# Performance work log

Hardware: AMD Instinct MI355X
Metric: run time of the kernel (lower is better)

## Reference

```python
import jax, jax.numpy as jnp
import numpy as np

DIM = 768
HEADS = 12
HEAD_DIM = DIM // HEADS
HIDDEN = int(DIM * 4.0)
EPS = 1e-5


def _layernorm(x, g, b):
    mu = jnp.mean(x, axis=-1, keepdims=True)
    var = jnp.var(x, axis=-1, keepdims=True)
    return (x - mu) * jax.lax.rsqrt(var + EPS) * g + b


def setup_inputs() -> dict:
    key = jax.random.key(0)
    ks = jax.random.split(key, 12)
    s = 0.02
    return {
        "x": jax.random.normal(ks[0], (8, 1024, DIM), dtype=jnp.float32),
        "norm1_g": jnp.ones((DIM,), jnp.float32),
        "norm1_b": jnp.zeros((DIM,), jnp.float32),
        "qkv_w": jax.random.normal(ks[1], (3 * DIM, DIM), jnp.float32) * s,
        "qkv_b": jnp.zeros((3 * DIM,), jnp.float32),
        "proj_w": jax.random.normal(ks[2], (DIM, DIM), jnp.float32) * s,
        "proj_b": jnp.zeros((DIM,), jnp.float32),
        "norm2_g": jnp.ones((DIM,), jnp.float32),
        "norm2_b": jnp.zeros((DIM,), jnp.float32),
        "fc1_w": jax.random.normal(ks[3], (HIDDEN, DIM), jnp.float32) * s,
        "fc1_b": jnp.zeros((HIDDEN,), jnp.float32),
        "fc2_w": jax.random.normal(ks[4], (DIM, HIDDEN), jnp.float32) * s,
        "fc2_b": jnp.zeros((DIM,), jnp.float32),
    }


def reference(x, norm1_g, norm1_b, qkv_w, qkv_b, proj_w, proj_b,
              norm2_g, norm2_b, fc1_w, fc1_b, fc2_w, fc2_b):
    B, N, C = x.shape
    scale = HEAD_DIM ** -0.5

    # --- MHSA with pre-norm + residual ---
    h = _layernorm(x, norm1_g, norm1_b)
    qkv = h @ qkv_w.T + qkv_b                      # [B, N, 3C]
    qkv = qkv.reshape(B, N, 3, HEADS, HEAD_DIM)
    qkv = jnp.transpose(qkv, (2, 0, 3, 1, 4))      # [3, B, H, N, Dh]
    q, k, v = qkv[0], qkv[1], qkv[2]
    attn = jnp.einsum("bhnd,bhmd->bhnm", q, k) * scale
    attn = jax.nn.softmax(attn, axis=-1)
    o = jnp.einsum("bhnm,bhmd->bhnd", attn, v)     # [B, H, N, Dh]
    o = jnp.transpose(o, (0, 2, 1, 3)).reshape(B, N, C)
    x = x + (o @ proj_w.T + proj_b)

    # --- MLP with pre-norm + residual ---
    h = _layernorm(x, norm2_g, norm2_b)
    h = jax.nn.gelu(h @ fc1_w.T + fc1_b, approximate=False)
    x = x + (h @ fc2_w.T + fc2_b)
    return x
```

## Files before the change

kernel.cpp:

```cpp
#include <hip/hip_runtime.h>
#include <hip/hip_bf16.h>

typedef unsigned short u16;
using short8  = __attribute__((ext_vector_type(8))) short;
using floatx4 = __attribute__((ext_vector_type(4))) float;

__device__ inline u16 f2bu(float f) {
    __hip_bfloat16 h = __float2bfloat16(f);
    return __builtin_bit_cast(u16, h);
}
__device__ inline float b2f(u16 u) {
    unsigned v = (unsigned)u << 16;
    return __builtin_bit_cast(float, v);
}
__device__ inline float gelu_f(float v) {
    float u = 1.5957691216f * (v + 0.044715f * v * v * v);
    return v / (1.f + __expf(-u));
}

__device__ inline void load16(const u16* g, u16* l) {
    __builtin_amdgcn_global_load_lds(
        (const __attribute__((address_space(1))) void*)g,
        (__attribute__((address_space(3))) void*)l, 16, 0, 0);
}

__global__ void cvt_bf16v(const float4* __restrict__ in, ushort4* __restrict__ out, int n4) {
    int i = blockIdx.x * 256 + threadIdx.x;
    if (i < n4) {
        float4 f = in[i];
        ushort4 r;
        r.x = f2bu(f.x); r.y = f2bu(f.y); r.z = f2bu(f.z); r.w = f2bu(f.w);
        out[i] = r;
    }
}

__global__ __launch_bounds__(256) void layernorm_bf16(
    const float* __restrict__ x, const float* __restrict__ g,
    const float* __restrict__ b, u16* __restrict__ out)
{
    int row = blockIdx.x;
    int tid = threadIdx.x;
    const float* xr = x + (size_t)row * 768;
    float v0 = xr[tid], v1 = xr[tid + 256], v2 = xr[tid + 512];
    float s = v0 + v1 + v2;
    float ss = v0 * v0 + v1 * v1 + v2 * v2;
    for (int off = 1; off < 64; off <<= 1) {
        s  += __shfl_xor(s, off, 64);
        ss += __shfl_xor(ss, off, 64);
    }
    __shared__ float as[4], ass[4];
    int wave = tid >> 6, lane = tid & 63;
    if (lane == 0) { as[wave] = s; ass[wave] = ss; }
    __syncthreads();
    s  = as[0] + as[1] + as[2] + as[3];
    ss = ass[0] + ass[1] + ass[2] + ass[3];
    float mu  = s * (1.0f / 768.0f);
    float var = ss * (1.0f / 768.0f) - mu * mu;
    float rs  = rsqrtf(var + 1e-5f);
    u16* orow = out + (size_t)row * 768;
    orow[tid]       = f2bu((v0 - mu) * rs * g[tid]       + b[tid]);
    orow[tid + 256] = f2bu((v1 - mu) * rs * g[tid + 256] + b[tid + 256]);
    orow[tid + 512] = f2bu((v2 - mu) * rs * g[tid + 512] + b[tid + 512]);
}

__global__ __launch_bounds__(256) void red2(
    const ushort4* __restrict__ P0, const ushort4* __restrict__ P1,
    const float* __restrict__ bias, const float4* __restrict__ res,
    float4* __restrict__ out)
{
    int i = blockIdx.x * 256 + threadIdx.x;
    int col = (i % 192) * 4;
    ushort4 a = P0[i], b = P1[i];
    float4 o = res ? res[i] : out[i];
    o.x += bias[col + 0] + b2f(a.x) + b2f(b.x);
    o.y += bias[col + 1] + b2f(a.y) + b2f(b.y);
    o.z += bias[col + 2] + b2f(a.z) + b2f(b.z);
    o.w += bias[col + 3] + b2f(a.w) + b2f(b.w);
    out[i] = o;
}

__device__ inline void mfma_tile(const u16* lsa, const u16* lsb, int off,
                                 int wrow, int wcol, int l16, int xq,
                                 floatx4 acc[4][4])
{
    short8 af[4], bfr[4];
    #pragma unroll
    for (int rb = 0; rb < 4; ++rb) af[rb]  = *(const short8*)&lsa[off + (wrow + rb * 16 + l16) * 32 + xq];
    #pragma unroll
    for (int cb = 0; cb < 4; ++cb) bfr[cb] = *(const short8*)&lsb[off + (wcol + cb * 16 + l16) * 32 + xq];
    #pragma unroll
    for (int rb = 0; rb < 4; ++rb)
        #pragma unroll
        for (int cb = 0; cb < 4; ++cb)
            acc[rb][cb] = __builtin_amdgcn_mfma_f32_16x16x32_bf16(af[rb], bfr[cb], acc[rb][cb], 0, 0, 0);
}

__global__ __launch_bounds__(256) void gemm_pipe(
    const u16* __restrict__ A, int lda,
    const u16* __restrict__ B, int ldb,
    int K,
    const float* __restrict__ bias,
    const float* __restrict__ res,
    float* __restrict__ outf, u16* __restrict__ outb,
    u16* __restrict__ parts, size_t pstride,
    int ldc, int act, int splits)
{
    __shared__ u16 lsa[2 * 128 * 32];
    __shared__ u16 lsb[2 * 128 * 32];

    int tid  = threadIdx.x;
    int wave = tid >> 6, lane = tid & 63;
    int quad = lane >> 4, l16 = lane & 15;
    int wrow = (wave >> 1) * 64;
    int wcol = (wave & 1) * 64;

    int gx = gridDim.x;
    int nblk = gx * gridDim.y;
    int flat = blockIdx.y * gx + blockIdx.x;
    int d = (flat & 7) * (nblk >> 3) + (flat >> 3);
    int m0 = (d / gx) * 128, n0 = (d % gx) * 128;

    int Kper = K / splits;
    int kbeg = blockIdx.z * Kper;
    int nIter = Kper >> 5;

    floatx4 acc[4][4];
    for (int i = 0; i < 4; ++i)
        for (int j = 0; j < 4; ++j)
            acc[i][j] = (floatx4){0.f, 0.f, 0.f, 0.f};

    int srow = wave * 32 + (lane >> 2);
    int scol = (((lane & 3) ^ ((lane >> 3) & 3))) * 8;
    const u16* ga0 = A + (size_t)(m0 + srow)      * lda + kbeg + scol;
    const u16* ga1 = A + (size_t)(m0 + srow + 16) * lda + kbeg + scol;
    const u16* gb0 = B + (size_t)(n0 + srow)      * ldb + kbeg + scol;
    const u16* gb1 = B + (size_t)(n0 + srow + 16) * ldb + kbeg + scol;
    int wl0 = wave * 1024 + lane * 8;
    int wl1 = wl0 + 512;

    int xq = (quad ^ ((l16 >> 1) & 3)) * 8;

    uint4 A00, A01, B00, B01;
    uint4 A10, A11, B10, B11;

#define FETCH0() do { A00 = *(const uint4*)ga0; A01 = *(const uint4*)ga1; \
                      B00 = *(const uint4*)gb0; B01 = *(const uint4*)gb1; \
                      ga0 += 32; ga1 += 32; gb0 += 32; gb1 += 32; } while (0)
#define FETCH1() do { A10 = *(const uint4*)ga0; A11 = *(const uint4*)ga1; \
                      B10 = *(const uint4*)gb0; B11 = *(const uint4*)gb1; \
                      ga0 += 32; ga1 += 32; gb0 += 32; gb1 += 32; } while (0)
#define WRITE0(buf) do { *(uint4*)&lsa[(buf) + wl0] = A00; *(uint4*)&lsa[(buf) + wl1] = A01; \
                         *(uint4*)&lsb[(buf) + wl0] = B00; *(uint4*)&lsb[(buf) + wl1] = B01; } while (0)
#define WRITE1(buf) do { *(uint4*)&lsa[(buf) + wl0] = A10; *(uint4*)&lsa[(buf) + wl1] = A11; \
                         *(uint4*)&lsb[(buf) + wl0] = B10; *(uint4*)&lsb[(buf) + wl1] = B11; } while (0)

    FETCH0();
    FETCH1();
    WRITE0(0);
    __syncthreads();

    for (int it = 0; it < nIter; it += 2) {
        if (it + 2 < nIter) FETCH0();
        mfma_tile(lsa, lsb, 0, wrow, wcol, l16, xq, acc);
        WRITE1(4096);
        __syncthreads();
        if (it + 3 < nIter) FETCH1();
        mfma_tile(lsa, lsb, 4096, wrow, wcol, l16, xq, acc);
        if (it + 2 < nIter) WRITE0(0);
        __syncthreads();
    }
#undef FETCH0
#undef FETCH1
#undef WRITE0
#undef WRITE1

    u16* pdst = (splits > 1) ? parts + (size_t)blockIdx.z * pstride : nullptr;
    #pragma unroll
    for (int rb = 0; rb < 4; ++rb)
        #pragma unroll
        for (int cb = 0; cb < 4; ++cb)
            #pragma unroll
            for (int r = 0; r < 4; ++r) {
                int row = m0 + wrow + rb * 16 + quad * 4 + r;
                int col = n0 + wcol + cb * 16 + l16;
                float v = acc[rb][cb][r];
                if (splits > 1) {
                    pdst[(size_t)row * ldc + col] = f2bu(v);
                } else {
                    v += bias[col];
                    if (res) v += res[(size_t)row * ldc + col];
                    if (act) v = gelu_f(v);
                    if (outf) outf[(size_t)row * ldc + col] = v;
                    else      outb[(size_t)row * ldc + col] = f2bu(v);
                }
            }
}

__global__ __launch_bounds__(256) void attn_fused(
    const u16* __restrict__ qkv, u16* __restrict__ o)
{
    const int N = 1024, C3 = 2304;
    int qb = blockIdx.x;
    int bh = blockIdx.y;
    int b = bh / 12, h = bh % 12;
    int tid = threadIdx.x, wave = tid >> 6, lane = tid & 63;
    int quad = lane >> 4, l16 = lane & 15;

    __shared__ u16 lk[64 * 64];
    __shared__ u16 lvt[64][72];
    __shared__ u16 lp[4][16][72];

    const size_t base = (size_t)b * N * C3;
    int q0 = qb * 64 + wave * 16;

    short8 qa0 = *(const short8*)&qkv[base + (size_t)(q0 + l16) * C3 + h * 64 + quad * 8];
    short8 qa1 = *(const short8*)&qkv[base + (size_t)(q0 + l16) * C3 + h * 64 + 32 + quad * 8];

    floatx4 oacc[4];
    for (int i = 0; i < 4; ++i) oacc[i] = (floatx4){0.f, 0.f, 0.f, 0.f};
    float lsum[4] = {0.f, 0.f, 0.f, 0.f};

    for (int kt = 0; kt < N; kt += 64) {
        __syncthreads();
        #pragma unroll
        for (int i = 0; i < 2; ++i) {
            int idx = i * 2048 + wave * 512 + lane * 8;
            int r = idx >> 6;
            int gc = (lane & 7) ^ (r & 7);
            load16(&qkv[base + (size_t)(kt + r) * C3 + 768 + h * 64 + gc * 8], &lk[idx]);
        }
        {
            int key = tid & 63, dbase = (tid >> 6) * 16;
            const u16* vp = &qkv[base + (size_t)(kt + key) * C3 + 1536 + h * 64 + dbase];
            uint4 vv0 = *(const uint4*)vp;
            uint4 vv1 = *(const uint4*)(vp + 8);
            const u16* e0 = (const u16*)&vv0;
            const u16* e1 = (const u16*)&vv1;
            #pragma unroll
            for (int i = 0; i < 8; ++i) {
                lvt[dbase + i][key]     = e0[i];
                lvt[dbase + 8 + i][key] = e1[i];
            }
        }
        __syncthreads();

        float p[4][4];
        #pragma unroll
        for (int kb = 0; kb < 4; ++kb) {
            int R = kb * 16 + l16;
            short8 b0 = *(short8*)&lk[R * 64 + ((quad ^ (R & 7)) * 8)];
            short8 b1 = *(short8*)&lk[R * 64 + (((quad + 4) ^ (R & 7)) * 8)];
            floatx4 c = (floatx4){0.f, 0.f, 0.f, 0.f};
            c = __builtin_amdgcn_mfma_f32_16x16x32_bf16(qa0, b0, c, 0, 0, 0);
            c = __builtin_amdgcn_mfma_f32_16x16x32_bf16(qa1, b1, c, 0, 0, 0);
            #pragma unroll
            for (int r = 0; r < 4; ++r) {
                p[kb][r] = __expf(c[r] * 0.125f);
                lsum[r] += p[kb][r];
            }
        }
        #pragma unroll
        for (int kb = 0; kb < 4; ++kb)
            #pragma unroll
            for (int r = 0; r < 4; ++r)
                lp[wave][quad * 4 + r][kb * 16 + l16] = f2bu(p[kb][r]);

        short8 pa0 = *(short8*)&lp[wave][l16][quad * 8];
        short8 pa1 = *(short8*)&lp[wave][l16][32 + quad * 8];
        #pragma unroll
        for (int db = 0; db < 4; ++db) {
            short8 vb0 = *(short8*)&lvt[db * 16 + l16][quad * 8];
            short8 vb1 = *(short8*)&lvt[db * 16 + l16][32 + quad * 8];
            oacc[db] = __builtin_amdgcn_mfma_f32_16x16x32_bf16(pa0, vb0, oacc[db], 0, 0, 0);
            oacc[db] = __builtin_amdgcn_mfma_f32_16x16x32_bf16(pa1, vb1, oacc[db], 0, 0, 0);
        }
    }

    #pragma unroll
    for (int r = 0; r < 4; ++r)
        for (int off = 1; off < 16; off <<= 1)
            lsum[r] += __shfl_xor(lsum[r], off, 64);

    #pragma unroll
    for (int db = 0; db < 4; ++db)
        #pragma unroll
        for (int r = 0; r < 4; ++r) {
            int row = q0 + quad * 4 + r;
            int col = h * 64 + db * 16 + l16;
            o[(size_t)(b * N + row) * 768 + col] = f2bu(oacc[db][r] / lsum[r]);
        }
}

extern "C" void kernel_launch(void* const* d_in, const int* in_sizes, int n_in,
                              void* d_out, int out_size, void* d_ws, size_t ws_size,
                              hipStream_t stream) {
    const float* x      = (const float*)d_in[0];
    const float* n1g    = (const float*)d_in[1];
    const float* n1b    = (const float*)d_in[2];
    const float* qkv_w  = (const float*)d_in[3];
    const float* qkv_b  = (const float*)d_in[4];
    const float* proj_w = (const float*)d_in[5];
    const float* proj_b = (const float*)d_in[6];
    const float* n2g    = (const float*)d_in[7];
    const float* n2b    = (const float*)d_in[8];
    const float* fc1_w  = (const float*)d_in[9];
    const float* fc1_b  = (const float*)d_in[10];
    const float* fc2_w  = (const float*)d_in[11];
    const float* fc2_b  = (const float*)d_in[12];
    float* out = (float*)d_out;

    const int T = 8192;
    char* ws = (char*)d_ws;
    u16* w_qkv  = (u16*)ws;               ws += (size_t)2304 * 768 * 2;
    u16* w_proj = (u16*)ws;               ws += (size_t)768 * 768 * 2;
    u16* w_fc1  = (u16*)ws;               ws += (size_t)3072 * 768 * 2;
    u16* w_fc2  = (u16*)ws;               ws += (size_t)768 * 3072 * 2;
    u16* h_buf  = (u16*)ws;               ws += (size_t)T * 768 * 2;
    u16* qkvbuf = (u16*)ws;               ws += (size_t)T * 2304 * 2;
    u16* o_buf  = (u16*)ws;               ws += (size_t)T * 768 * 2;
    u16* pbuf   = (u16*)ws;               ws += (size_t)T * 768 * 2;
    u16* fc1out = qkvbuf;
    bool do_split = (size_t)(ws - (char*)d_ws) <= ws_size;
    size_t pstr = (size_t)(pbuf - h_buf);

    cvt_bf16v<<<dim3(2304 * 768 / 4 / 256), 256, 0, stream>>>((const float4*)qkv_w,  (ushort4*)w_qkv,  2304 * 768 / 4);
    cvt_bf16v<<<dim3(768 * 768 / 4 / 256),  256, 0, stream>>>((const float4*)proj_w, (ushort4*)w_proj, 768 * 768 / 4);
    cvt_bf16v<<<dim3(3072 * 768 / 4 / 256), 256, 0, stream>>>((const float4*)fc1_w,  (ushort4*)w_fc1,  3072 * 768 / 4);
    cvt_bf16v<<<dim3(768 * 3072 / 4 / 256), 256, 0, stream>>>((const float4*)fc2_w,  (ushort4*)w_fc2,  768 * 3072 / 4);

    layernorm_bf16<<<dim3(T), 256, 0, stream>>>(x, n1g, n1b, h_buf);
    gemm_pipe<<<dim3(2304 / 128, T / 128), 256, 0, stream>>>(
        h_buf, 768, w_qkv, 768, 768, qkv_b, nullptr, nullptr, qkvbuf, nullptr, 0, 2304, 0, 1);
    attn_fused<<<dim3(16, 96), 256, 0, stream>>>(qkvbuf, o_buf);
    if (do_split) {
        gemm_pipe<<<dim3(768 / 128, T / 128, 2), 256, 0, stream>>>(
            o_buf, 768, w_proj, 768, 768, proj_b, nullptr, nullptr, nullptr,
            h_buf, pstr, 768, 0, 2);
        red2<<<dim3(T * 768 / 4 / 256), 256, 0, stream>>>(
            (const ushort4*)h_buf, (const ushort4*)pbuf, proj_b, (const float4*)x, (float4*)out);
    } else {
        gemm_pipe<<<dim3(768 / 128, T / 128), 256, 0, stream>>>(
            o_buf, 768, w_proj, 768, 768, proj_b, x, out, nullptr, nullptr, 0, 768, 0, 1);
    }
    layernorm_bf16<<<dim3(T), 256, 0, stream>>>(out, n2g, n2b, h_buf);
    gemm_pipe<<<dim3(3072 / 128, T / 128), 256, 0, stream>>>(
        h_buf, 768, w_fc1, 768, 768, fc1_b, nullptr, nullptr, fc1out, nullptr, 0, 3072, 1, 1);
    if (do_split) {
        gemm_pipe<<<dim3(768 / 128, T / 128, 2), 256, 0, stream>>>(
            fc1out, 3072, w_fc2, 3072, 3072, fc2_b, nullptr, nullptr, nullptr,
            h_buf, pstr, 768, 0, 2);
        red2<<<dim3(T * 768 / 4 / 256), 256, 0, stream>>>(
            (const ushort4*)h_buf, (const ushort4*)pbuf, fc2_b, nullptr, (float4*)out);
    } else {
        gemm_pipe<<<dim3(768 / 128, T / 128), 256, 0, stream>>>(
            fc1out, 3072, w_fc2, 3072, 3072, fc2_b, out, out, nullptr, nullptr, 0, 768, 0, 1);
    }
}
```

Before: 427.2 us.

## Replace register-staged double-buffered GEMM with single-buffer direct-to-LDS loads

The GEMM no longer prefetches tiles into registers and double-buffers them in LDS. Each K step now issues global_load_lds to copy the tile straight into one LDS buffer, separated by two barriers, and launch bounds ask for 6 blocks per CU. The aim is to cut register pressure and LDS footprint so more waves fit per CU, letting occupancy hide memory latency instead of explicit software pipelining. The cost is that loads no longer overlap with MFMA inside a block, and there are two barriers per 32-wide K step.

```diff
diff --git a/kernel.cpp b/kernel.cpp
--- a/kernel.cpp
+++ b/kernel.cpp
@@ -79,23 +79,7 @@
     out[i] = o;
 }
 
-__device__ inline void mfma_tile(const u16* lsa, const u16* lsb, int off,
-                                 int wrow, int wcol, int l16, int xq,
-                                 floatx4 acc[4][4])
-{
-    short8 af[4], bfr[4];
-    #pragma unroll
-    for (int rb = 0; rb < 4; ++rb) af[rb]  = *(const short8*)&lsa[off + (wrow + rb * 16 + l16) * 32 + xq];
-    #pragma unroll
-    for (int cb = 0; cb < 4; ++cb) bfr[cb] = *(const short8*)&lsb[off + (wcol + cb * 16 + l16) * 32 + xq];
-    #pragma unroll
-    for (int rb = 0; rb < 4; ++rb)
-        #pragma unroll
-        for (int cb = 0; cb < 4; ++cb)
-            acc[rb][cb] = __builtin_amdgcn_mfma_f32_16x16x32_bf16(af[rb], bfr[cb], acc[rb][cb], 0, 0, 0);
-}
-
-__global__ __launch_bounds__(256) void gemm_pipe(
+__global__ __launch_bounds__(256, 6) void gemm_lds(
     const u16* __restrict__ A, int lda,
     const u16* __restrict__ B, int ldb,
     int K,
@@ -105,8 +89,8 @@
     u16* __restrict__ parts, size_t pstride,
     int ldc, int act, int splits)
 {
-    __shared__ u16 lsa[2 * 128 * 32];
-    __shared__ u16 lsb[2 * 128 * 32];
+    __shared__ u16 lsa[128 * 32];
+    __shared__ u16 lsb[128 * 32];
 
     int tid  = threadIdx.x;
     int wave = tid >> 6, lane = tid & 63;
@@ -122,7 +106,6 @@
 
     int Kper = K / splits;
     int kbeg = blockIdx.z * Kper;
-    int nIter = Kper >> 5;
 
     floatx4 acc[4][4];
     for (int i = 0; i < 4; ++i)
@@ -135,44 +118,30 @@
     const u16* ga1 = A + (size_t)(m0 + srow + 16) * lda + kbeg + scol;
     const u16* gb0 = B + (size_t)(n0 + srow)      * ldb + kbeg + scol;
     const u16* gb1 = B + (size_t)(n0 + srow + 16) * ldb + kbeg + scol;
-    int wl0 = wave * 1024 + lane * 8;
-    int wl1 = wl0 + 512;
+    int lofs = wave * 1024;
 
     int xq = (quad ^ ((l16 >> 1) & 3)) * 8;
 
-    uint4 A00, A01, B00, B01;
-    uint4 A10, A11, B10, B11;
-
-#define FETCH0() do { A00 = *(const uint4*)ga0; A01 = *(const uint4*)ga1; \
-                      B00 = *(const uint4*)gb0; B01 = *(const uint4*)gb1; \
-                      ga0 += 32; ga1 += 32; gb0 += 32; gb1 += 32; } while (0)
-#define FETCH1() do { A10 = *(const uint4*)ga0; A11 = *(const uint4*)ga1; \
-                      B10 = *(const uint4*)gb0; B11 = *(const uint4*)gb1; \
-                      ga0 += 32; ga1 += 32; gb0 += 32; gb1 += 32; } while (0)
-#define WRITE0(buf) do { *(uint4*)&lsa[(buf) + wl0] = A00; *(uint4*)&lsa[(buf) + wl1] = A01; \
-                         *(uint4*)&lsb[(buf) + wl0] = B00; *(uint4*)&lsb[(buf) + wl1] = B01; } while (0)
-#define WRITE1(buf) do { *(uint4*)&lsa[(buf) + wl0] = A10; *(uint4*)&lsa[(buf) + wl1] = A11; \
-                         *(uint4*)&lsb[(buf) + wl0] = B10; *(uint4*)&lsb[(buf) + wl1] = B11; } while (0)
-
-    FETCH0();
-    FETCH1();
-    WRITE0(0);
-    __syncthreads();
-
-    for (int it = 0; it < nIter; it += 2) {
-        if (it + 2 < nIter) FETCH0();
-        mfma_tile(lsa, lsb, 0, wrow, wcol, l16, xq, acc);
-        WRITE1(4096);
+    for (int k0 = 0; k0 < Kper; k0 += 32) {
         __syncthreads();
-        if (it + 3 < nIter) FETCH1();
-        mfma_tile(lsa, lsb, 4096, wrow, wcol, l16, xq, acc);
-        if (it + 2 < nIter) WRITE0(0);
+        load16(ga0, &lsa[lofs]);
+        load16(ga1, &lsa[lofs + 512]);
+        load16(gb0, &lsb[lofs]);
+        load16(gb1, &lsb[lofs + 512]);
+        ga0 += 32; ga1 += 32; gb0 += 32; gb1 += 32;
         __syncthreads();
-    }
-#undef FETCH0
-#undef FETCH1
-#undef WRITE0
-#undef WRITE1
+
+        short8 af[4], bfr[4];
+        #pragma unroll
+        for (int rb = 0; rb < 4; ++rb) af[rb]  = *(short8*)&lsa[(wrow + rb * 16 + l16) * 32 + xq];
+        #pragma unroll
+        for (int cb = 0; cb < 4; ++cb) bfr[cb] = *(short8*)&lsb[(wcol + cb * 16 + l16) * 32 + xq];
+        #pragma unroll
+        for (int rb = 0; rb < 4; ++rb)
+            #pragma unroll
+            for (int cb = 0; cb < 4; ++cb)
+                acc[rb][cb] = __builtin_amdgcn_mfma_f32_16x16x32_bf16(af[rb], bfr[cb], acc[rb][cb], 0, 0, 0);
+    }
 
     u16* pdst = (splits > 1) ? parts + (size_t)blockIdx.z * pstride : nullptr;
     #pragma unroll
@@ -329,30 +298,30 @@
     cvt_bf16v<<<dim3(768 * 3072 / 4 / 256), 256, 0, stream>>>((const float4*)fc2_w,  (ushort4*)w_fc2,  768 * 3072 / 4);
 
     layernorm_bf16<<<dim3(T), 256, 0, stream>>>(x, n1g, n1b, h_buf);
-    gemm_pipe<<<dim3(2304 / 128, T / 128), 256, 0, stream>>>(
+    gemm_lds<<<dim3(2304 / 128, T / 128), 256, 0, stream>>>(
         h_buf, 768, w_qkv, 768, 768, qkv_b, nullptr, nullptr, qkvbuf, nullptr, 0, 2304, 0, 1);
     attn_fused<<<dim3(16, 96), 256, 0, stream>>>(qkvbuf, o_buf);
     if (do_split) {
-        gemm_pipe<<<dim3(768 / 128, T / 128, 2), 256, 0, stream>>>(
+        gemm_lds<<<dim3(768 / 128, T / 128, 2), 256, 0, stream>>>(
             o_buf, 768, w_proj, 768, 768, proj_b, nullptr, nullptr, nullptr,
             h_buf, pstr, 768, 0, 2);
         red2<<<dim3(T * 768 / 4 / 256), 256, 0, stream>>>(
             (const ushort4*)h_buf, (const ushort4*)pbuf, proj_b, (const float4*)x, (float4*)out);
     } else {
-        gemm_pipe<<<dim3(768 / 128, T / 128), 256, 0, stream>>>(
+        gemm_lds<<<dim3(768 / 128, T / 128), 256, 0, stream>>>(
             o_buf, 768, w_proj, 768, 768, proj_b, x, out, nullptr, nullptr, 0, 768, 0, 1);
     }
     layernorm_bf16<<<dim3(T), 256, 0, stream>>>(out, n2g, n2b, h_buf);
-    gemm_pipe<<<dim3(3072 / 128, T / 128), 256, 0, stream>>>(
+    gemm_lds<<<dim3(3072 / 128, T / 128), 256, 0, stream>>>(
         h_buf, 768, w_fc1, 768, 768, fc1_b, nullptr, nullptr, fc1out, nullptr, 0, 3072, 1, 1);
     if (do_split) {
-        gemm_pipe<<<dim3(768 / 128, T / 128, 2), 256, 0, stream>>>(
+        gemm_lds<<<dim3(768 / 128, T / 128, 2), 256, 0, stream>>>(
             fc1out, 3072, w_fc2, 3072, 3072, fc2_b, nullptr, nullptr, nullptr,
             h_buf, pstr, 768, 0, 2);
         red2<<<dim3(T * 768 / 4 / 256), 256, 0, stream>>>(
             (const ushort4*)h_buf, (const ushort4*)pbuf, fc2_b, nullptr, (float4*)out);
     } else {
-        gemm_pipe<<<dim3(768 / 128, T / 128), 256, 0, stream>>>(
+        gemm_lds<<<dim3(768 / 128, T / 128), 256, 0, stream>>>(
             fc1out, 3072, w_fc2, 3072, 3072, fc2_b, out, out, nullptr, nullptr, 0, 768, 0, 1);
     }
 }
```

Measured after the change: 977.7 us. 2.29x slower.
